# Optimization experiments

Hardware: AMD Instinct MI355X
Metric: run time of the kernel (lower is better)

## Reference

```python
import jax, jax.numpy as jnp
import numpy as np

D = 2048
NH = 16
DH = D // NH          # 128
DC = D // 4           # 512  (KV latent)
DCQ = D // 2          # 1024 (Q latent)
B = 1
L = 2048
MAX_LEN = 4096


def precompute_rope(dh, max_len):
    inv_freq = 1.0 / (10000.0 ** (jnp.arange(0, dh, 2, dtype=jnp.float32) / dh))
    t = jnp.arange(max_len, dtype=jnp.float32)
    freqs = jnp.outer(t, inv_freq)                 # [max_len, dh/2]
    emb = jnp.concatenate([freqs, freqs], axis=-1) # [max_len, dh]
    return jnp.cos(emb), jnp.sin(emb)


def apply_rope(t, cos, sin):
    # t: [B, H, L, dh]; cos/sin: [L, dh]
    x1, x2 = jnp.split(t, 2, axis=-1)
    rot = jnp.concatenate([-x2, x1], axis=-1)
    return t * cos + rot * sin


def setup_inputs() -> dict:
    key = jax.random.key(0)
    ks = jax.random.split(key, 9)
    s = 0.02
    return {
        "x": jax.random.normal(ks[0], (B, L, D), dtype=jnp.float32),
        "W_DKV": jax.random.normal(ks[1], (D, DC), dtype=jnp.float32) * s,
        "W_UK": jax.random.normal(ks[2], (DC, NH * DH), dtype=jnp.float32) * s,
        "W_UV": jax.random.normal(ks[3], (DC, NH * DH), dtype=jnp.float32) * s,
        "W_DQ": jax.random.normal(ks[4], (D, DCQ), dtype=jnp.float32) * s,
        "W_UQ": jax.random.normal(ks[5], (DCQ, 2 * NH * DH), dtype=jnp.float32) * s,
        "W_lam": jax.random.normal(ks[6], (D, NH), dtype=jnp.float32) * s,
        "b_lam": jnp.zeros((NH,), dtype=jnp.float32),
        "W_out": jax.random.normal(ks[7], (D, D), dtype=jnp.float32) * s,
    }


def reference(x, W_DKV, W_UK, W_UV, W_DQ, W_UQ, W_lam, b_lam, W_out):
    Bx, Lx, Dx = x.shape
    cos, sin = precompute_rope(DH, MAX_LEN)
    cos, sin = cos[:Lx], sin[:Lx]

    # MLA KV compression: single K/V shared by the paired query heads
    c_kv = x @ W_DKV                                            # [B, L, dc]
    k = (c_kv @ W_UK).reshape(Bx, Lx, NH, DH).transpose(0, 2, 1, 3)   # [B, nh, L, dh]
    v = (c_kv @ W_UV).reshape(Bx, Lx, NH, DH).transpose(0, 2, 1, 3)   # [B, nh, L, dh]

    # Low-rank Q, doubled heads for differential attention
    c_q = x @ W_DQ                                              # [B, L, dcq]
    q = (c_q @ W_UQ).reshape(Bx, Lx, 2 * NH, DH).transpose(0, 2, 1, 3)  # [B, 2nh, L, dh]

    q = apply_rope(q, cos, sin)
    k = apply_rope(k, cos, sin)

    # Group paired heads (2i, 2i+1) share k/v head i -> avoid repeat_interleave
    qp = q.reshape(Bx, NH, 2, Lx, DH)                           # [B, nh, 2, L, dh]
    scale = 1.0 / jnp.sqrt(jnp.asarray(DH, dtype=x.dtype))
    scores = jnp.einsum('bhpqd,bhkd->bhpqk', qp, k) * scale     # [B, nh, 2, L, L]
    causal = jnp.tril(jnp.ones((Lx, Lx), dtype=bool))
    scores = jnp.where(causal, scores, jnp.asarray(-jnp.inf, dtype=scores.dtype))
    probs = jax.nn.softmax(scores, axis=-1)
    attn = jnp.einsum('bhpqk,bhkd->bhpqd', probs, v)            # [B, nh, 2, L, dh]
    attn1, attn2 = attn[:, :, 0], attn[:, :, 1]                 # [B, nh, L, dh]

    # Token-specific sigmoid lambda per head
    lam = jax.nn.sigmoid(x @ W_lam + b_lam)                     # [B, L, nh]
    lam = lam.transpose(0, 2, 1)[..., None]                     # [B, nh, L, 1]

    out = (attn1 - lam * attn2).transpose(0, 2, 1, 3).reshape(Bx, Lx, Dx)
    return out @ W_out
```

## Files before the change

kernel.cpp:

```cpp
#include <hip/hip_runtime.h>
#include <cstdint>
#include <cstddef>

typedef __bf16 bf16x8 __attribute__((ext_vector_type(8)));
typedef __bf16 bf16x4 __attribute__((ext_vector_type(4)));
typedef float f32x4 __attribute__((ext_vector_type(4)));


template <int N> __device__ __forceinline__ void waitcnt_vm() {
  if constexpr (N == 3)      asm volatile("s_waitcnt vmcnt(3)" ::: "memory");
  else if constexpr (N == 4) asm volatile("s_waitcnt vmcnt(4)" ::: "memory");
  else if constexpr (N == 6) asm volatile("s_waitcnt vmcnt(6)" ::: "memory");
  else if constexpr (N == 8) asm volatile("s_waitcnt vmcnt(8)" ::: "memory");
  else                       asm volatile("s_waitcnt vmcnt(0)" ::: "memory");
}

template <int BM, int NKS>
__device__ __forceinline__ void gemm_core(const __bf16* __restrict__ A,
                                          const __bf16* __restrict__ Bt,
                                          int K, int bm, int bn,
                                          __bf16* As, __bf16* Bs,
                                          f32x4 (*acc)[4]) {
  const int tid = threadIdx.x;
  const int w = tid >> 6;
  const int lane = tid & 63;
  const int quad = lane >> 4;
  const int l16 = lane & 15;
  constexpr int WM = (BM == 128) ? 64 : 32;
  constexpr int MI = WM / 16;
  constexpr int NL = NKS * (BM / 64 + 2);
  const int wm = (w & 1) * WM;
  const int wn = (w >> 1) * 64;
  const int srow = lane >> 2;
  const int sseg = (lane & 3) * 8;

  auto stage = [&](int k0, int buf) {
#pragma unroll
    for (int ks = 0; ks < NKS; ++ks) {
#pragma unroll
      for (int g = 0; g < BM / 64; ++g) {
        const int grp = w + g * 4;
        const __bf16* ga = A + (size_t)(bm + grp * 16 + srow) * K + k0 + ks * 32 + sseg;
        __builtin_amdgcn_global_load_lds(
            (const __attribute__((address_space(1))) void*)ga,
            (__attribute__((address_space(3))) void*)&As[(buf * NKS + ks) * (BM * 32) + grp * 512],
            16, 0, 0);
      }
#pragma unroll
      for (int g = 0; g < 2; ++g) {
        const int grp = w + g * 4;
        const __bf16* gb = Bt + (size_t)(bn + grp * 16 + srow) * K + k0 + ks * 32 + sseg;
        __builtin_amdgcn_global_load_lds(
            (const __attribute__((address_space(1))) void*)gb,
            (__attribute__((address_space(3))) void*)&Bs[(buf * NKS + ks) * 4096 + grp * 512],
            16, 0, 0);
      }
    }
  };

#pragma unroll
  for (int i = 0; i < MI; ++i)
#pragma unroll
    for (int j = 0; j < 4; ++j) acc[i][j] = (f32x4){0.f, 0.f, 0.f, 0.f};

  asm volatile("s_waitcnt vmcnt(0)" ::: "memory");
  stage(0, 0);

  const int NIT = K / (32 * NKS);
  for (int it = 0; it < NIT; ++it) {
    const int cur = it & 1;
    if (it + 1 < NIT) {
      stage((it + 1) * 32 * NKS, cur ^ 1);
      waitcnt_vm<NL>();
    } else {
      waitcnt_vm<0>();
    }
    __builtin_amdgcn_s_barrier();
    asm volatile("" ::: "memory");
    const __bf16* Ab = &As[cur * NKS * (BM * 32)];
    const __bf16* Bb = &Bs[cur * NKS * 4096];
#pragma unroll
    for (int ks = 0; ks < NKS; ++ks) {
      bf16x8 af[MI], bfr[4];
#pragma unroll
      for (int i = 0; i < MI; ++i)
        af[i] = *(const bf16x8*)&Ab[ks * (BM * 32) + (wm + i * 16 + l16) * 32 + quad * 8];
#pragma unroll
      for (int j = 0; j < 4; ++j)
        bfr[j] = *(const bf16x8*)&Bb[ks * 4096 + (wn + j * 16 + l16) * 32 + quad * 8];
#pragma unroll
      for (int i = 0; i < MI; ++i)
#pragma unroll
        for (int j = 0; j < 4; ++j)
          acc[i][j] = __builtin_amdgcn_mfma_f32_16x16x32_bf16(af[i], bfr[j],
                                                              acc[i][j], 0, 0, 0);
    }
    asm volatile("s_waitcnt lgkmcnt(0)" ::: "memory");
    __builtin_amdgcn_s_barrier();
    asm volatile("" ::: "memory");
  }
}

template <int BM, int NKS, bool BF16OUT>
__device__ __forceinline__ void gemm_body(const __bf16* __restrict__ A,
                                          const __bf16* __restrict__ Bt,
                                          void* __restrict__ Cv,
                                          int N, int K, int bm, int bn,
                                          __bf16* As, __bf16* Bs) {
  constexpr int MI = (BM == 128) ? 4 : 2;
  constexpr int WM = (BM == 128) ? 64 : 32;
  f32x4 acc[MI][4];
  gemm_core<BM, NKS>(A, Bt, K, bm, bn, As, Bs, acc);
  const int tid = threadIdx.x;
  const int w = tid >> 6, lane = tid & 63, quad = lane >> 4, l16 = lane & 15;
  const int wm = (w & 1) * WM, wn = (w >> 1) * 64;
#pragma unroll
  for (int i = 0; i < MI; ++i)
#pragma unroll
    for (int j = 0; j < 4; ++j)
#pragma unroll
      for (int r = 0; r < 4; ++r) {
        const int row = bm + wm + i * 16 + quad * 4 + r;
        const int col = bn + wn + j * 16 + l16;
        if constexpr (BF16OUT)
          ((__bf16*)Cv)[(size_t)row * N + col] = (__bf16)acc[i][j][r];
        else
          ((float*)Cv)[(size_t)row * N + col] = acc[i][j][r];
      }
}

template <int BM, int NKS, bool BF16OUT>
__global__ __launch_bounds__(256) void gemm_mfma(const __bf16* __restrict__ A,
                                                 const __bf16* __restrict__ Bt,
                                                 void* __restrict__ Cv,
                                                 int M, int N, int K) {
  __shared__ __bf16 As[2 * BM * 32 * NKS];
  __shared__ __bf16 Bs[2 * 128 * 32 * NKS];
  gemm_body<BM, NKS, BF16OUT>(A, Bt, Cv, N, K, blockIdx.y * BM, blockIdx.x * 128, As, Bs);
}

__global__ __launch_bounds__(256) void down_lam(
    const __bf16* __restrict__ x_bf, const __bf16* __restrict__ WtDKV,
    const __bf16* __restrict__ WtDQ, __bf16* __restrict__ c_kv,
    __bf16* __restrict__ c_q, const __bf16* __restrict__ WlT,
    const float* __restrict__ b_lam, float* __restrict__ lam) {
  __shared__ __bf16 As[2 * 64 * 32 * 2];
  __shared__ __bf16 Bs[2 * 128 * 32 * 2];
  const int bx = blockIdx.x;
  const int tid = threadIdx.x;
  if (bx == 12) {
    const int w = tid >> 6, lane = tid & 63, quad = lane >> 4, l16 = lane & 15;
    const int m0 = (blockIdx.y * 4 + w) * 16;
    const __bf16* xrow = x_bf + (size_t)(m0 + l16) * 2048 + quad * 8;
    const __bf16* wrow = WlT + (size_t)l16 * 2048 + quad * 8;
    f32x4 acc[4];
#pragma unroll
    for (int u = 0; u < 4; ++u) acc[u] = (f32x4){0.f, 0.f, 0.f, 0.f};
    for (int k0 = 0; k0 < 2048; k0 += 128) {
#pragma unroll
      for (int u = 0; u < 4; ++u) {
        bf16x8 a = *(const bf16x8*)&xrow[k0 + u * 32];
        bf16x8 b = *(const bf16x8*)&wrow[k0 + u * 32];
        acc[u] = __builtin_amdgcn_mfma_f32_16x16x32_bf16(a, b, acc[u], 0, 0, 0);
      }
    }
    const float bl = b_lam[l16];
#pragma unroll
    for (int r = 0; r < 4; ++r) {
      const float v = acc[0][r] + acc[1][r] + acc[2][r] + acc[3][r] + bl;
      lam[(size_t)(m0 + quad * 4 + r) * 16 + l16] = 1.0f / (1.0f + __expf(-v));
    }
    return;
  }
  if (bx < 4)
    gemm_body<64, 2, true>(x_bf, WtDKV, (void*)c_kv, 512, 2048,
                           blockIdx.y * 64, bx * 128, As, Bs);
  else
    gemm_body<64, 2, true>(x_bf, WtDQ, (void*)c_q, 1024, 2048,
                           blockIdx.y * 64, (bx - 4) * 128, As, Bs);
}

__global__ __launch_bounds__(256) void up_fused3(
    const __bf16* __restrict__ c_kv, const __bf16* __restrict__ WtUK,
    const __bf16* __restrict__ WtUV, const __bf16* __restrict__ c_q,
    const __bf16* __restrict__ WtUQ, __bf16* __restrict__ k_bf,
    __bf16* __restrict__ v_t, __bf16* __restrict__ q_bf,
    const float* __restrict__ cosT, const float* __restrict__ sinT) {
  __shared__ __align__(16) char usm[32768];
  __bf16* As = (__bf16*)usm;
  __bf16* Bs = (__bf16*)(usm + 16384);
  const int bx = blockIdx.x;
  const int bm = blockIdx.y * 128;
  const int tid = threadIdx.x;
  const int w = tid >> 6, lane = tid & 63, quad = lane >> 4, l16 = lane & 15;
  const int wm = (w & 1) * 64, wn = (w >> 1) * 64;
  f32x4 acc[4][4];
  if (bx < 16) {
    const int bn = bx * 128;
    gemm_core<128, 1>(c_kv, WtUK, 512, bm, bn, As, Bs, acc);
    __bf16 (*Kt)[128] = (__bf16(*)[128])usm;
#pragma unroll
    for (int i = 0; i < 4; ++i)
#pragma unroll
      for (int j = 0; j < 4; ++j)
#pragma unroll
        for (int r = 0; r < 4; ++r)
          Kt[wm + i * 16 + quad * 4 + r][wn + j * 16 + l16] = (__bf16)acc[i][j][r];
    __syncthreads();
#pragma unroll
    for (int j = 0; j < 4; ++j) {
      const int d = wn + j * 16 + l16;
      const float sgn = (d < 64) ? -1.f : 1.f;
#pragma unroll
      for (int i = 0; i < 4; ++i)
#pragma unroll
        for (int r = 0; r < 4; ++r) {
          const int lr = wm + i * 16 + quad * 4 + r;
          const int l = bm + lr;
          const float v = (float)Kt[lr][d];
          const float pr = (float)Kt[lr][d ^ 64];
          const float ov = v * cosT[l * 128 + d] + sgn * pr * sinT[l * 128 + d];
          k_bf[(size_t)l * 2048 + bn + d] = (__bf16)ov;
        }
    }
  } else if (bx < 32) {
    const int bn = (bx - 16) * 128;
    gemm_core<128, 1>(c_kv, WtUV, 512, bm, bn, As, Bs, acc);
#pragma unroll
    for (int i = 0; i < 4; ++i)
#pragma unroll
      for (int j = 0; j < 4; ++j) {
        const int d = bn + wn + j * 16 + l16;
        const int l = bm + wm + i * 16 + quad * 4;
        bf16x4 pk = {(__bf16)acc[i][j][0], (__bf16)acc[i][j][1],
                     (__bf16)acc[i][j][2], (__bf16)acc[i][j][3]};
        *(bf16x4*)&v_t[(size_t)d * 2048 + l] = pk;
      }
  } else {
    const int bn = (bx - 32) * 128;
    gemm_core<128, 1>(c_q, WtUQ, 1024, bm, bn, As, Bs, acc);
#pragma unroll
    for (int i = 0; i < 4; ++i)
#pragma unroll
      for (int j = 0; j < 4; ++j)
#pragma unroll
        for (int r = 0; r < 4; ++r) {
          const int row = bm + wm + i * 16 + quad * 4 + r;
          const int col = bn + wn + j * 16 + l16;
          q_bf[(size_t)row * 4096 + col] = (__bf16)acc[i][j][r];
        }
  }
}

__global__ __launch_bounds__(256) void prep_all(
    const float* __restrict__ W_DKV, const float* __restrict__ W_DQ,
    const float* __restrict__ W_UK,  const float* __restrict__ W_UV,
    const float* __restrict__ W_UQ,
    const float* __restrict__ x,     const float* __restrict__ W_lam,
    __bf16* __restrict__ tDKV, __bf16* __restrict__ tDQ,
    __bf16* __restrict__ tUK,  __bf16* __restrict__ tUV,
    __bf16* __restrict__ tUQ,
    __bf16* __restrict__ x_bf, __bf16* __restrict__ WlT,
    float* __restrict__ cosT, float* __restrict__ sinT) {
  __shared__ float T[32][36];
  int t = blockIdx.x;
  const int tid = threadIdx.x;
  if (t < 9216) {
    const float* src; __bf16* dst; int K, N, kx, ny;
    if (t < 1024)      {            src = W_DKV; dst = tDKV; K = 2048; N = 512;  kx = t & 63; ny = t >> 6; }
    else if (t < 3072) { t -= 1024; src = W_DQ;  dst = tDQ;  K = 2048; N = 1024; kx = t & 63; ny = t >> 6; }
    else if (t < 4096) { t -= 3072; src = W_UK;  dst = tUK;  K = 512;  N = 2048; kx = t & 15; ny = t >> 4; }
    else if (t < 5120) { t -= 4096; src = W_UV;  dst = tUV;  K = 512;  N = 2048; kx = t & 15; ny = t >> 4; }
    else               { t -= 5120; src = W_UQ;  dst = tUQ;  K = 1024; N = 4096; kx = t & 31; ny = t >> 5; }
    const int k0 = kx * 32;
    const int n0 = ny * 32;
    const int r = tid >> 3;
    const int c = (tid & 7) * 4;
    *(float4*)&T[r][c] = *(const float4*)&src[(size_t)(k0 + r) * N + n0 + c];
    __syncthreads();
    bf16x4 o = {(__bf16)T[c + 0][r], (__bf16)T[c + 1][r],
                (__bf16)T[c + 2][r], (__bf16)T[c + 3][r]};
    *(bf16x4*)&dst[(size_t)(n0 + r) * K + k0 + c] = o;
    return;
  }
  t -= 9216;
  if (t < 4096) {
    const int i = t * 256 + tid;
    float4 v = *(const float4*)&x[(size_t)i * 4];
    bf16x4 o = {(__bf16)v.x, (__bf16)v.y, (__bf16)v.z, (__bf16)v.w};
    *(bf16x4*)&x_bf[(size_t)i * 4] = o;
    return;
  }
  t -= 4096;
  if (t < 1024) {
    const int l = t * 2 + (tid >> 7);
    const int d = tid & 127;
    const int j = d & 63;
    const float inv = exp2f(-(float)j * 0.2076205059304601f);
    const float ang = (float)l * inv;
    cosT[l * 128 + d] = cosf(ang);
    sinT[l * 128 + d] = sinf(ang);
    return;
  }
  t -= 1024;
  {
    const int i = t * 256 + tid;
    const int k = i >> 4, n = i & 15;
    WlT[(size_t)n * 2048 + k] = (__bf16)W_lam[i];
  }
}

__global__ __launch_bounds__(512, 2) void attn_kernel3(
    const __bf16* __restrict__ Qb, const __bf16* __restrict__ Kb,
    const __bf16* __restrict__ Vt, const float* __restrict__ cosT,
    const float* __restrict__ sinT, const float* __restrict__ lam,
    __bf16* __restrict__ y, const float* __restrict__ W_out,
    __bf16* __restrict__ Wt_out) {
  __shared__ __align__(16) char smem[81920];
  float (*Ex)[132] = (float(*)[132])smem;

  const int bx = blockIdx.x;
  const int tid = threadIdx.x;
  if (bx >= 512) {
    const int t = (bx - 512) * 2 + (tid >> 8);
    const int st = tid & 255;
    float (*T)[36] = (float(*)[36])(smem + (tid >> 8) * 4608);
    const int k0 = (t & 63) * 32;
    const int n0 = (t >> 6) * 32;
    const int r = st >> 3;
    const int c = (st & 7) * 4;
    *(float4*)&T[r][c] = *(const float4*)&W_out[(size_t)(k0 + r) * 2048 + n0 + c];
    __syncthreads();
    bf16x4 o = {(__bf16)T[c + 0][r], (__bf16)T[c + 1][r],
                (__bf16)T[c + 2][r], (__bf16)T[c + 3][r]};
    *(bf16x4*)&Wt_out[(size_t)(n0 + r) * 2048 + k0 + c] = o;
    return;
  }
  const int hv = bx >> 8;
  const int ii = bx & 255;
  const int qt = hv ? (ii >> 4) : 31 - (ii >> 4);
  const int hk = ii & 15;
  const int q0 = qt * 64;
  const int w = tid >> 6, lane = tid & 63, quad = lane >> 4, l16 = lane & 15;
  const int wrow = (w & 3) * 16;
  const int qoff = (2 * hk + (w >> 2)) * 128;
  const int kvoff = hk * 128;
  const float qscale = 0.08838834764831845f;
  char* Pw = smem + 65536 + w * 2048;

  bf16x8 aq[4];
  {
    const int l = q0 + wrow + l16;
    const size_t qbase = (size_t)l * 4096 + qoff + quad * 8;
    bf16x8 raw[4];
#pragma unroll
    for (int ks = 0; ks < 4; ++ks)
      raw[ks] = *(const bf16x8*)&Qb[qbase + ks * 32];
#pragma unroll
    for (int ks = 0; ks < 4; ++ks) {
      const float* cp = &cosT[l * 128 + ks * 32 + quad * 8];
      const float* sp = &sinT[l * 128 + ks * 32 + quad * 8];
#pragma unroll
      for (int j = 0; j < 8; ++j) {
        const float cv = cp[j];
        const float sv = sp[j];
        const float rot = (ks < 2) ? -(float)raw[ks + 2][j] : (float)raw[ks - 2][j];
        aq[ks][j] = (__bf16)(((float)raw[ks][j] * cv + rot * sv) * qscale);
      }
    }
  }

  auto stage = [&](int kt_, char* buf) {
    const int k0_ = kt_ * 64;
    __bf16* Ksb = (__bf16*)buf;
    __bf16* Vsb = (__bf16*)(buf + 16384);
#pragma unroll
    for (int d = 0; d < 2; ++d) {
      const int r0 = w * 8 + d * 4;
      const int row = r0 + (lane >> 4);
      const int ck = (lane & 15) ^ (row & 15);
      const __bf16* ga = Kb + (size_t)(k0_ + row) * 2048 + kvoff + ck * 8;
      __builtin_amdgcn_global_load_lds(
          (const __attribute__((address_space(1))) void*)ga,
          (__attribute__((address_space(3))) void*)&Ksb[r0 * 128], 16, 0, 0);
      const int r0v = w * 16 + d * 8;
      const int rowv = r0v + (lane >> 3);
      const int cv = (lane & 7) ^ (rowv & 7);
      const __bf16* gv = Vt + (size_t)(kvoff + rowv) * 2048 + k0_ + cv * 8;
      __builtin_amdgcn_global_load_lds(
          (const __attribute__((address_space(1))) void*)gv,
          (__attribute__((address_space(3))) void*)&Vsb[r0v * 64], 16, 0, 0);
    }
  };

  f32x4 o[8];
#pragma unroll
  for (int i = 0; i < 8; ++i) o[i] = (f32x4){0.f, 0.f, 0.f, 0.f};
  float m = -1e30f, lsum = 0.f;

  asm volatile("s_waitcnt vmcnt(0)" ::: "memory");
  stage(0, smem);

  for (int kt = 0; kt <= qt; ++kt) {
    const int cur = kt & 1;
    __bf16* Ks = (__bf16*)(smem + cur * 32768);
    __bf16* Vs = (__bf16*)(smem + cur * 32768 + 16384);
    const int k0 = kt * 64;
    if (kt < qt) {
      stage(kt + 1, smem + (cur ^ 1) * 32768);
      asm volatile("s_waitcnt vmcnt(4)" ::: "memory");
    } else {
      asm volatile("s_waitcnt vmcnt(0)" ::: "memory");
    }
    __builtin_amdgcn_s_barrier();
    asm volatile("" ::: "memory");
    f32x4 st[4];
#pragma unroll
    for (int t = 0; t < 4; ++t) st[t] = (f32x4){0.f, 0.f, 0.f, 0.f};
    __builtin_amdgcn_s_setprio(1);
#pragma unroll
    for (int ks = 0; ks < 4; ++ks) {
#pragma unroll
      for (int t = 0; t < 4; ++t) {
        bf16x8 ak = *(bf16x8*)&Ks[(t * 16 + l16) * 128 + (((ks * 4 + quad) ^ l16) << 3)];
        st[t] = __builtin_amdgcn_mfma_f32_16x16x32_bf16(ak, aq[ks], st[t], 0, 0, 0);
      }
    }
    __builtin_amdgcn_s_setprio(0);
    {
      const int q = q0 + wrow + l16;
      float rm = -1e30f;
      if (kt != qt) {
#pragma unroll
        for (int t = 0; t < 4; ++t)
#pragma unroll
          for (int r = 0; r < 4; ++r) rm = fmaxf(rm, st[t][r]);
      } else {
#pragma unroll
        for (int t = 0; t < 4; ++t)
#pragma unroll
          for (int r = 0; r < 4; ++r) {
            const int key = k0 + t * 16 + quad * 4 + r;
            if (key > q) st[t][r] = -1e30f;
            rm = fmaxf(rm, st[t][r]);
          }
      }
      rm = fmaxf(rm, __shfl_xor(rm, 16, 64));
      rm = fmaxf(rm, __shfl_xor(rm, 32, 64));
      const float mn = fmaxf(m, rm);
      float rs = 0.f;
#pragma unroll
      for (int t = 0; t < 4; ++t)
#pragma unroll
        for (int r = 0; r < 4; ++r) {
          st[t][r] = __expf(st[t][r] - mn);
          rs += st[t][r];
        }
      rs += __shfl_xor(rs, 16, 64);
      rs += __shfl_xor(rs, 32, 64);
      if (__any(rm > m)) {
        const float alpha = __expf(m - mn);
        lsum = lsum * alpha + rs;
        m = mn;
#pragma unroll
        for (int r = 0; r < 4; ++r) {
          const float ar = __shfl(alpha, quad * 4 + r, 64);
#pragma unroll
          for (int nt = 0; nt < 8; ++nt) o[nt][r] *= ar;
        }
      } else {
        lsum += rs;
      }
      const int prow = l16;
#pragma unroll
      for (int t = 0; t < 4; ++t) {
        bf16x4 pk = {(__bf16)st[t][0], (__bf16)st[t][1],
                     (__bf16)st[t][2], (__bf16)st[t][3]};
        const int wch = (t * 2 + (quad >> 1)) ^ (prow & 7);
        *(bf16x4*)(Pw + prow * 128 + wch * 16 + (quad & 1) * 8) = pk;
      }
    }
    __builtin_amdgcn_s_setprio(1);
#pragma unroll
    for (int ks = 0; ks < 2; ++ks) {
      const int rch = ((ks * 4 + quad) ^ (l16 & 7)) << 4;
      bf16x8 pa = *(bf16x8*)(Pw + l16 * 128 + rch);
#pragma unroll
      for (int nt = 0; nt < 8; ++nt) {
        bf16x8 bv = *(bf16x8*)&Vs[(nt * 16 + l16) * 64 + (((ks * 4 + quad) ^ (l16 & 7)) << 3)];
        o[nt] = __builtin_amdgcn_mfma_f32_16x16x32_bf16(pa, bv, o[nt], 0, 0, 0);
      }
    }
    __builtin_amdgcn_s_setprio(0);
    asm volatile("s_waitcnt lgkmcnt(0)" ::: "memory");
    __builtin_amdgcn_s_barrier();
    asm volatile("" ::: "memory");
  }
  const float linv = 1.0f / lsum;
  if (w >= 4) {
#pragma unroll
    for (int r = 0; r < 4; ++r) {
      const float inv = __shfl(linv, quad * 4 + r, 64);
      const int rr = wrow + quad * 4 + r;
#pragma unroll
      for (int nt = 0; nt < 8; ++nt)
        Ex[rr][nt * 16 + l16] = o[nt][r] * inv;
    }
  }
  __syncthreads();
  if (w < 4) {
#pragma unroll
    for (int r = 0; r < 4; ++r) {
      const float inv = __shfl(linv, quad * 4 + r, 64);
      const int rr = wrow + quad * 4 + r;
      const int l = q0 + rr;
      const float lm = lam[l * 16 + hk];
      __bf16* dst = y + (size_t)l * 2048 + hk * 128;
#pragma unroll
      for (int nt = 0; nt < 8; ++nt) {
        const float v1 = o[nt][r] * inv;
        dst[nt * 16 + l16] = (__bf16)(v1 - lm * Ex[rr][nt * 16 + l16]);
      }
    }
  }
}

extern "C" void kernel_launch(void* const* d_in, const int* in_sizes, int n_in,
                              void* d_out, int out_size, void* d_ws, size_t ws_size,
                              hipStream_t stream) {
  const float* x     = (const float*)d_in[0];
  const float* W_DKV = (const float*)d_in[1];
  const float* W_UK  = (const float*)d_in[2];
  const float* W_UV  = (const float*)d_in[3];
  const float* W_DQ  = (const float*)d_in[4];
  const float* W_UQ  = (const float*)d_in[5];
  const float* W_lam = (const float*)d_in[6];
  const float* b_lam = (const float*)d_in[7];
  const float* W_out = (const float*)d_in[8];
  float* out = (float*)d_out;

  char* ws = (char*)d_ws;
  #define MB(n) ((size_t)(n) << 20)
  __bf16* x_bf   = (__bf16*)(ws + MB(0));
  __bf16* Wt_DKV = (__bf16*)(ws + MB(8));
  __bf16* Wt_DQ  = (__bf16*)(ws + MB(10));
  __bf16* c_kv   = (__bf16*)(ws + MB(14));
  __bf16* c_q    = (__bf16*)(ws + MB(16));
  __bf16* Wt_UK  = (__bf16*)(ws + MB(20));
  __bf16* Wt_UV  = (__bf16*)(ws + MB(22));
  __bf16* Wt_UQ  = (__bf16*)(ws + MB(24));
  __bf16* k_bf   = (__bf16*)(ws + MB(32));
  __bf16* y_bf   = (__bf16*)(ws + MB(40));
  __bf16* q_bf   = (__bf16*)(ws + MB(48));
  __bf16* v_t    = (__bf16*)(ws + MB(64));
  float*  lam    = (float*)(ws + MB(88));
  float*  cosT   = (float*)(ws + MB(89));
  float*  sinT   = (float*)(ws + MB(90));
  __bf16* WlT    = (__bf16*)(ws + MB(91));
  __bf16* Wt_out = (__bf16*)(ws + MB(92));

  prep_all<<<14464, 256, 0, stream>>>(W_DKV, W_DQ, W_UK, W_UV, W_UQ,
                                      x, W_lam,
                                      Wt_DKV, Wt_DQ, Wt_UK, Wt_UV, Wt_UQ,
                                      x_bf, WlT, cosT, sinT);
  down_lam<<<dim3(13, 32), 256, 0, stream>>>(x_bf, Wt_DKV, Wt_DQ, c_kv, c_q,
                                             WlT, b_lam, lam);
  up_fused3<<<dim3(64, 16), 256, 0, stream>>>(c_kv, Wt_UK, Wt_UV, c_q, Wt_UQ,
                                              k_bf, v_t, q_bf, cosT, sinT);
  attn_kernel3<<<2560, 512, 0, stream>>>(q_bf, k_bf, v_t, cosT, sinT, lam,
                                         y_bf, W_out, Wt_out);
  gemm_mfma<64, 2, false><<<dim3(16, 32), 256, 0, stream>>>(y_bf, Wt_out, out, 2048, 2048, 2048);
}
```

Baseline: 300.5 us.

## Move up-projection weight transposes and RoPE tables into down-projection kernel

The W_UK/W_UV/W_UQ fp32-to-bf16 transposes and the cos/sin table generation move out of the prep kernel and become extra blocks appended to the down-projection/lambda kernel, which now uses a flattened 1D grid. The prep kernel shrinks to the work the down GEMM actually depends on. The goal is to overlap this independent prep work with the down-projection GEMM and shorten the critical prep stage. The added blocks are scheduled after the GEMM blocks, so they may mostly fill tail slots, and they compete with the GEMM for bandwidth.

```diff
diff --git a/kernel.cpp b/kernel.cpp
--- a/kernel.cpp
+++ b/kernel.cpp
@@ -139,45 +139,92 @@
   gemm_body<BM, NKS, BF16OUT>(A, Bt, Cv, N, K, blockIdx.y * BM, blockIdx.x * 128, As, Bs);
 }
 
+__device__ __forceinline__ void transpose_tile(const float* __restrict__ src,
+                                               __bf16* __restrict__ dst,
+                                               int K, int N, int kx, int ny,
+                                               float (*T)[36], int tid) {
+  const int k0 = kx * 32;
+  const int n0 = ny * 32;
+  const int r = tid >> 3;
+  const int c = (tid & 7) * 4;
+  *(float4*)&T[r][c] = *(const float4*)&src[(size_t)(k0 + r) * N + n0 + c];
+  __syncthreads();
+  bf16x4 o = {(__bf16)T[c + 0][r], (__bf16)T[c + 1][r],
+              (__bf16)T[c + 2][r], (__bf16)T[c + 3][r]};
+  *(bf16x4*)&dst[(size_t)(n0 + r) * K + k0 + c] = o;
+}
+
 __global__ __launch_bounds__(256) void down_lam(
     const __bf16* __restrict__ x_bf, const __bf16* __restrict__ WtDKV,
     const __bf16* __restrict__ WtDQ, __bf16* __restrict__ c_kv,
     __bf16* __restrict__ c_q, const __bf16* __restrict__ WlT,
-    const float* __restrict__ b_lam, float* __restrict__ lam) {
+    const float* __restrict__ b_lam, float* __restrict__ lam,
+    const float* __restrict__ W_UK, const float* __restrict__ W_UV,
+    const float* __restrict__ W_UQ, __bf16* __restrict__ tUK,
+    __bf16* __restrict__ tUV, __bf16* __restrict__ tUQ,
+    float* __restrict__ cosT, float* __restrict__ sinT) {
   __shared__ __bf16 As[2 * 64 * 32 * 2];
   __shared__ __bf16 Bs[2 * 128 * 32 * 2];
-  const int bx = blockIdx.x;
+  int id = blockIdx.x;
   const int tid = threadIdx.x;
-  if (bx == 12) {
-    const int w = tid >> 6, lane = tid & 63, quad = lane >> 4, l16 = lane & 15;
-    const int m0 = (blockIdx.y * 4 + w) * 16;
-    const __bf16* xrow = x_bf + (size_t)(m0 + l16) * 2048 + quad * 8;
-    const __bf16* wrow = WlT + (size_t)l16 * 2048 + quad * 8;
-    f32x4 acc[4];
-#pragma unroll
-    for (int u = 0; u < 4; ++u) acc[u] = (f32x4){0.f, 0.f, 0.f, 0.f};
-    for (int k0 = 0; k0 < 2048; k0 += 128) {
-#pragma unroll
-      for (int u = 0; u < 4; ++u) {
-        bf16x8 a = *(const bf16x8*)&xrow[k0 + u * 32];
-        bf16x8 b = *(const bf16x8*)&wrow[k0 + u * 32];
-        acc[u] = __builtin_amdgcn_mfma_f32_16x16x32_bf16(a, b, acc[u], 0, 0, 0);
-      }
-    }
-    const float bl = b_lam[l16];
-#pragma unroll
-    for (int r = 0; r < 4; ++r) {
-      const float v = acc[0][r] + acc[1][r] + acc[2][r] + acc[3][r] + bl;
-      lam[(size_t)(m0 + quad * 4 + r) * 16 + l16] = 1.0f / (1.0f + __expf(-v));
-    }
+  if (id < 416) {
+    const int bxl = id >> 5, by = id & 31;
+    if (bxl == 12) {
+      const int w = tid >> 6, lane = tid & 63, quad = lane >> 4, l16 = lane & 15;
+      const int m0 = (by * 4 + w) * 16;
+      const __bf16* xrow = x_bf + (size_t)(m0 + l16) * 2048 + quad * 8;
+      const __bf16* wrow = WlT + (size_t)l16 * 2048 + quad * 8;
+      f32x4 acc[4];
+#pragma unroll
+      for (int u = 0; u < 4; ++u) acc[u] = (f32x4){0.f, 0.f, 0.f, 0.f};
+      for (int k0 = 0; k0 < 2048; k0 += 128) {
+#pragma unroll
+        for (int u = 0; u < 4; ++u) {
+          bf16x8 a = *(const bf16x8*)&xrow[k0 + u * 32];
+          bf16x8 b = *(const bf16x8*)&wrow[k0 + u * 32];
+          acc[u] = __builtin_amdgcn_mfma_f32_16x16x32_bf16(a, b, acc[u], 0, 0, 0);
+        }
+      }
+      const float bl = b_lam[l16];
+#pragma unroll
+      for (int r = 0; r < 4; ++r) {
+        const float v = acc[0][r] + acc[1][r] + acc[2][r] + acc[3][r] + bl;
+        lam[(size_t)(m0 + quad * 4 + r) * 16 + l16] = 1.0f / (1.0f + __expf(-v));
+      }
+      return;
+    }
+    if (bxl < 4)
+      gemm_body<64, 2, true>(x_bf, WtDKV, (void*)c_kv, 512, 2048,
+                             by * 64, bxl * 128, As, Bs);
+    else
+      gemm_body<64, 2, true>(x_bf, WtDQ, (void*)c_q, 1024, 2048,
+                             by * 64, (bxl - 4) * 128, As, Bs);
     return;
   }
-  if (bx < 4)
-    gemm_body<64, 2, true>(x_bf, WtDKV, (void*)c_kv, 512, 2048,
-                           blockIdx.y * 64, bx * 128, As, Bs);
-  else
-    gemm_body<64, 2, true>(x_bf, WtDQ, (void*)c_q, 1024, 2048,
-                           blockIdx.y * 64, (bx - 4) * 128, As, Bs);
+  id -= 416;
+  if (id < 6144) {
+    float (*T)[36] = (float(*)[36])As;
+    if (id < 1024)
+      transpose_tile(W_UK, tUK, 512, 2048, id & 15, id >> 4, T, tid);
+    else if (id < 2048) {
+      id -= 1024;
+      transpose_tile(W_UV, tUV, 512, 2048, id & 15, id >> 4, T, tid);
+    } else {
+      id -= 2048;
+      transpose_tile(W_UQ, tUQ, 1024, 4096, id & 31, id >> 5, T, tid);
+    }
+    return;
+  }
+  id -= 6144;
+  {
+    const int l = id * 2 + (tid >> 7);
+    const int d = tid & 127;
+    const int j = d & 63;
+    const float inv = exp2f(-(float)j * 0.2076205059304601f);
+    const float ang = (float)l * inv;
+    cosT[l * 128 + d] = cosf(ang);
+    sinT[l * 128 + d] = sinf(ang);
+  }
 }
 
 __global__ __launch_bounds__(256) void up_fused3(
@@ -254,36 +301,22 @@
 
 __global__ __launch_bounds__(256) void prep_all(
     const float* __restrict__ W_DKV, const float* __restrict__ W_DQ,
-    const float* __restrict__ W_UK,  const float* __restrict__ W_UV,
-    const float* __restrict__ W_UQ,
     const float* __restrict__ x,     const float* __restrict__ W_lam,
     __bf16* __restrict__ tDKV, __bf16* __restrict__ tDQ,
-    __bf16* __restrict__ tUK,  __bf16* __restrict__ tUV,
-    __bf16* __restrict__ tUQ,
-    __bf16* __restrict__ x_bf, __bf16* __restrict__ WlT,
-    float* __restrict__ cosT, float* __restrict__ sinT) {
+    __bf16* __restrict__ x_bf, __bf16* __restrict__ WlT) {
   __shared__ float T[32][36];
   int t = blockIdx.x;
   const int tid = threadIdx.x;
-  if (t < 9216) {
-    const float* src; __bf16* dst; int K, N, kx, ny;
-    if (t < 1024)      {            src = W_DKV; dst = tDKV; K = 2048; N = 512;  kx = t & 63; ny = t >> 6; }
-    else if (t < 3072) { t -= 1024; src = W_DQ;  dst = tDQ;  K = 2048; N = 1024; kx = t & 63; ny = t >> 6; }
-    else if (t < 4096) { t -= 3072; src = W_UK;  dst = tUK;  K = 512;  N = 2048; kx = t & 15; ny = t >> 4; }
-    else if (t < 5120) { t -= 4096; src = W_UV;  dst = tUV;  K = 512;  N = 2048; kx = t & 15; ny = t >> 4; }
-    else               { t -= 5120; src = W_UQ;  dst = tUQ;  K = 1024; N = 4096; kx = t & 31; ny = t >> 5; }
-    const int k0 = kx * 32;
-    const int n0 = ny * 32;
-    const int r = tid >> 3;
-    const int c = (tid & 7) * 4;
-    *(float4*)&T[r][c] = *(const float4*)&src[(size_t)(k0 + r) * N + n0 + c];
-    __syncthreads();
-    bf16x4 o = {(__bf16)T[c + 0][r], (__bf16)T[c + 1][r],
-                (__bf16)T[c + 2][r], (__bf16)T[c + 3][r]};
-    *(bf16x4*)&dst[(size_t)(n0 + r) * K + k0 + c] = o;
+  if (t < 3072) {
+    if (t < 1024)
+      transpose_tile(W_DKV, tDKV, 2048, 512, t & 63, t >> 6, T, tid);
+    else {
+      t -= 1024;
+      transpose_tile(W_DQ, tDQ, 2048, 1024, t & 63, t >> 6, T, tid);
+    }
     return;
   }
-  t -= 9216;
+  t -= 3072;
   if (t < 4096) {
     const int i = t * 256 + tid;
     float4 v = *(const float4*)&x[(size_t)i * 4];
@@ -292,17 +325,6 @@
     return;
   }
   t -= 4096;
-  if (t < 1024) {
-    const int l = t * 2 + (tid >> 7);
-    const int d = tid & 127;
-    const int j = d & 63;
-    const float inv = exp2f(-(float)j * 0.2076205059304601f);
-    const float ang = (float)l * inv;
-    cosT[l * 128 + d] = cosf(ang);
-    sinT[l * 128 + d] = sinf(ang);
-    return;
-  }
-  t -= 1024;
   {
     const int i = t * 256 + tid;
     const int k = i >> 4, n = i & 15;
@@ -559,12 +581,12 @@
   __bf16* WlT    = (__bf16*)(ws + MB(91));
   __bf16* Wt_out = (__bf16*)(ws + MB(92));
 
-  prep_all<<<14464, 256, 0, stream>>>(W_DKV, W_DQ, W_UK, W_UV, W_UQ,
-                                      x, W_lam,
-                                      Wt_DKV, Wt_DQ, Wt_UK, Wt_UV, Wt_UQ,
-                                      x_bf, WlT, cosT, sinT);
-  down_lam<<<dim3(13, 32), 256, 0, stream>>>(x_bf, Wt_DKV, Wt_DQ, c_kv, c_q,
-                                             WlT, b_lam, lam);
+  prep_all<<<7296, 256, 0, stream>>>(W_DKV, W_DQ, x, W_lam,
+                                     Wt_DKV, Wt_DQ, x_bf, WlT);
+  down_lam<<<7584, 256, 0, stream>>>(x_bf, Wt_DKV, Wt_DQ, c_kv, c_q,
+                                     WlT, b_lam, lam,
+                                     W_UK, W_UV, W_UQ, Wt_UK, Wt_UV, Wt_UQ,
+                                     cosT, sinT);
   up_fused3<<<dim3(64, 16), 256, 0, stream>>>(c_kv, Wt_UK, Wt_UV, c_q, Wt_UQ,
                                               k_bf, v_t, q_bf, cosT, sinT);
   attn_kernel3<<<2560, 512, 0, stream>>>(q_bf, k_bf, v_t, cosT, sinT, lam,
```

After: 288.4 us. 1.04x faster.
